# Kernel optimization log

Hardware: AMD Instinct MI355X
Metric: run time of the kernel (lower is better)

Reference implementation:

```python
import jax, jax.numpy as jnp
import numpy as np

CHEB = jnp.array([676.5203681218851, -1259.1392167224028, 771.3234287776531,
                  -176.6150291621406, 12.507343278686905, -0.13857109526572012,
                  9.984369578019572e-06, 1.5056327351493116e-07], dtype=jnp.float32)
TWO_PI = float(np.sqrt(2.0 * np.pi))  # sqrt(2*pi), matches torch two_pi constant


def _gamma(z):
    # Lanczos approximation, 8 Chebyshev terms
    x = jnp.full_like(z, 0.9999999999998099)
    for i in range(8):
        x = x + CHEB[i] / (z + (i + 1.0))
    t = z + 8.0 - 0.5
    y = TWO_PI * t ** (z + 0.5) * jnp.exp(-t) * x
    return y / z


def _lower_incl_gamma(s, x, iters=8):
    it = iters - 2
    gs = _gamma(s)
    L = x ** s * gs * jnp.exp(-x)
    gs = gs * s
    R = jnp.reciprocal(gs) * jnp.ones_like(x)
    X = x
    for k in range(it):
        gs = gs * (s + k + 1)
        R = R + X / gs
        X = X * x
    gs = gs * (s + it + 1)
    R = R + X / gs
    return L * R


def _trigamma(x):
    z = x + 1.0
    zz = z * z
    a = 0.2 - jnp.reciprocal(7.0 * zz)
    b = 1.0 - a / zz
    c = 1.0 + b / (3.0 * z)
    d = 1.0 + c / (2.0 * z)
    return d / z + jnp.reciprocal(x * x)


def _k_update(k, s):
    nm = jnp.log(k) - jax.scipy.special.digamma(k) - s
    dn = jnp.reciprocal(k) - _trigamma(k)
    return k - nm / dn


def _compute_ml_est(x, i=10):
    # x: [B, N]; returns per-image k, th of shape [B]
    x = x + 1e-07
    mean_x = jnp.mean(x, axis=1)
    s = jnp.log(mean_x) - jnp.mean(jnp.log(x), axis=1)
    s3 = s - 3.0
    rt = jnp.sqrt(s3 * s3 + 24.0 * s)
    k = (3.0 - s + rt) / (12.0 * s) + 1e-07
    for _ in range(i):
        k = _k_update(k, s)
    k = jnp.clip(k, 1e-07, 18.0)
    th = jnp.reciprocal(k) * mean_x
    return k, th


def setup_inputs() -> dict:
    key = jax.random.key(0)
    x = jax.random.uniform(key, (256, 224, 224), dtype=jnp.float32)
    return {"x": x}


def reference(x):
    B, H, W = x.shape
    xf = x.reshape(B, H * W)
    xf = xf - jnp.min(xf, axis=1, keepdims=True) + 1e-07
    k, th = _compute_ml_est(xf)            # [B], [B]
    kb = k[:, None]                         # broadcast per-image stats over pixels
    y = jnp.reciprocal(_gamma(kb)) * _lower_incl_gamma(kb, xf / th[:, None])
    y = jnp.where(jnp.isfinite(y), y, jnp.zeros_like(y))
    return y.reshape(B, H, W)
```

## Files before the change

### kernel.cpp

```cpp
#include <hip/hip_runtime.h>
#include <math.h>

#define HW   50176
#define NV4  12544
#define TPB  1024

typedef float floatx4 __attribute__((ext_vector_type(4)));

__device__ __forceinline__ float waveMin(float v) {
#pragma unroll
    for (int o = 32; o > 0; o >>= 1) v = fminf(v, __shfl_down(v, o, 64));
    return v;
}
__device__ __forceinline__ double waveSumD(double v) {
#pragma unroll
    for (int o = 32; o > 0; o >>= 1) v += __shfl_down(v, o, 64);
    return v;
}

__device__ __forceinline__ float digamma_f(float x) {
    float r = 0.0f;
#pragma unroll 6
    for (int i = 0; i < 6; ++i) {
        if (x < 6.0f) { r -= __fdividef(1.0f, x); x += 1.0f; }
    }
    float f = __fdividef(1.0f, x * x);
    float ser = f * (1.0f/12.0f - f * (1.0f/120.0f - f * (1.0f/252.0f - f * (1.0f/240.0f - f * (1.0f/132.0f)))));
    return r + logf(x) - 0.5f * __fdividef(1.0f, x) - ser;
}
__device__ __forceinline__ float trigamma_ref(float x) {
    float z = x + 1.0f, zz = z * z;
    float a = 0.2f - __fdividef(1.0f, 7.0f * zz);
    float b = 1.0f - __fdividef(a, zz);
    float c = 1.0f + __fdividef(b, 3.0f * z);
    float d = 1.0f + __fdividef(c, 2.0f * z);
    return __fdividef(d, z) + __fdividef(1.0f, x * x);
}

__global__ void __launch_bounds__(TPB)
gamma_norm2d(const float* __restrict__ x, float* __restrict__ out) {
    const int row = blockIdx.x;
    const int tid = threadIdx.x;
    const float4* __restrict__ xr = (const float4*)(x + (size_t)row * HW);

    const bool extra = (tid < (NV4 - 12 * TPB));

    float4 v[13];
#pragma unroll
    for (int j = 0; j < 12; ++j) v[j] = xr[tid + j * TPB];
    v[12] = extra ? xr[tid + 12 * TPB]
                  : make_float4(INFINITY, INFINITY, INFINITY, INFINITY);

    float pmin = INFINITY, psum = 0.0f;
#pragma unroll
    for (int j = 0; j < 13; ++j) {
        pmin = fminf(pmin, fminf(fminf(v[j].x, v[j].y), fminf(v[j].z, v[j].w)));
        if (j < 12 || extra) psum += (v[j].x + v[j].y) + (v[j].z + v[j].w);
    }
    pmin = waveMin(pmin);
    double dsum = waveSumD((double)psum);

    __shared__ float  smin[16];
    __shared__ double sacc[16];
    __shared__ float  sparams[3];
    __shared__ float  scoef[8];

    const int wid = tid >> 6, lane = tid & 63;
    if (lane == 0) { smin[wid] = pmin; sacc[wid] = dsum; }
    __syncthreads();
    if (tid == 0) {
        float mm = smin[0];
        for (int i = 1; i < 16; ++i) mm = fminf(mm, smin[i]);
        sparams[0] = mm;
    }
    __syncthreads();
    const float rmin = sparams[0];

    float psl = 0.0f;
#pragma unroll
    for (int j = 0; j < 13; ++j) {
        if (j < 12 || extra) {
            psl += (__logf(v[j].x - rmin + 1e-7f + 1e-7f) + __logf(v[j].y - rmin + 1e-7f + 1e-7f))
                 + (__logf(v[j].z - rmin + 1e-7f + 1e-7f) + __logf(v[j].w - rmin + 1e-7f + 1e-7f));
        }
    }
    double dsl = waveSumD((double)psl);
    __shared__ double ssl[16];
    if (lane == 0) ssl[wid] = dsl;
    __syncthreads();

    if (tid == 0) {
        double ts = 0.0, tl = 0.0;
        for (int i = 0; i < 16; ++i) { ts += sacc[i]; tl += ssl[i]; }
        ts -= (double)HW * ((double)rmin - 2e-7);
        const double meand = ts / (double)HW;
        float s = logf((float)meand) - (float)(tl / (double)HW);

        float s3 = s - 3.0f;
        float rt = sqrtf(s3 * s3 + 24.0f * s);
        float k  = __fdividef(3.0f - s + rt, 12.0f * s) + 1e-7f;
#pragma unroll
        for (int it = 0; it < 10; ++it) {
            float nm = logf(k) - digamma_f(k) - s;
            float dn = __fdividef(1.0f, k) - trigamma_ref(k);
            k -= __fdividef(nm, dn);
        }
        if (k < 1e-7f) k = 1e-7f;
        if (k > 18.0f) k = 18.0f;

        const double CH[8] = {676.5203681218851, -1259.1392167224028, 771.3234287776531,
                              -176.6150291621406, 12.507343278686905, -0.13857109526572012,
                              9.984369578019572e-06, 1.5056327351493116e-07};
        double acc = 0.9999999999998099;
#pragma unroll
        for (int i = 0; i < 8; ++i) acc += CH[i] / ((double)k + (double)(i + 1));
        float t  = k + 7.5f;
        float g  = __expf(fmaf(k + 0.5f, __logf(t), -t)) * 2.50662827463f * (float)acc / k;

        float den = g * k;
        scoef[0] = __fdividef(1.0f, den);
#pragma unroll
        for (int j = 1; j < 8; ++j) {
            den *= (k + (float)j);
            scoef[j] = __fdividef(1.0f, den);
        }
        sparams[1] = k;
        sparams[2] = (float)((double)k / meand);
    }
    __syncthreads();

    const float kk = sparams[1], invth = sparams[2];
    const float c0 = scoef[0], c1 = scoef[1], c2 = scoef[2], c3 = scoef[3];
    const float c4 = scoef[4], c5 = scoef[5], c6 = scoef[6], c7 = scoef[7];

    floatx4* __restrict__ yr = (floatx4*)(out + (size_t)row * HW);
#pragma unroll
    for (int j = 0; j < 13; ++j) {
        if (j < 12 || extra) {
            float e[4] = {v[j].x, v[j].y, v[j].z, v[j].w};
            floatx4 o;
#pragma unroll
            for (int q = 0; q < 4; ++q) {
                float xq = (e[q] - rmin + 1e-7f) * invth;
                float p = fmaf(c7, xq, c6);
                p = fmaf(p, xq, c5);
                p = fmaf(p, xq, c4);
                p = fmaf(p, xq, c3);
                p = fmaf(p, xq, c2);
                p = fmaf(p, xq, c1);
                p = fmaf(p, xq, c0);
                float y = __expf(fmaf(kk, __logf(xq), -xq)) * p;
                o[q] = isfinite(y) ? y : 0.0f;
            }
            __builtin_nontemporal_store(o, yr + tid + j * TPB);
        }
    }
}

extern "C" void kernel_launch(void* const* d_in, const int* in_sizes, int n_in,
                              void* d_out, int out_size, void* d_ws, size_t ws_size,
                              hipStream_t stream) {
    const float* x = (const float*)d_in[0];
    float* out = (float*)d_out;
    const int rows = in_sizes[0] / HW;
    gamma_norm2d<<<dim3(rows), dim3(TPB), 0, stream>>>(x, out);
}
```

Baseline: 110.7 us.

## Cut per-element log work, drop a barrier, and trim Newton iterations

Every thread now reduces the per-wave minima itself, which removes one __syncthreads and a shared-memory round trip. The log-sum takes one log2 of the product of four shifted values instead of four natural logs. The final pass folds the shift and scale into one fma and works in base 2 with exp2/log2. Newton iterations for k drop from 10 to 6 and the logs use fast intrinsics. The risks are overflow or underflow of the four-way product and a less converged k, both of which could change the output.

```diff
diff --git a/kernel.cpp b/kernel.cpp
--- a/kernel.cpp
+++ b/kernel.cpp
@@ -26,7 +26,7 @@
     }
     float f = __fdividef(1.0f, x * x);
     float ser = f * (1.0f/12.0f - f * (1.0f/120.0f - f * (1.0f/252.0f - f * (1.0f/240.0f - f * (1.0f/132.0f)))));
-    return r + logf(x) - 0.5f * __fdividef(1.0f, x) - ser;
+    return r + __logf(x) - 0.5f * __fdividef(1.0f, x) - ser;
 }
 __device__ __forceinline__ float trigamma_ref(float x) {
     float z = x + 1.0f, zz = z * z;
@@ -62,46 +62,45 @@
 
     __shared__ float  smin[16];
     __shared__ double sacc[16];
-    __shared__ float  sparams[3];
+    __shared__ double ssl[16];
+    __shared__ float  sparams[2];
     __shared__ float  scoef[8];
 
     const int wid = tid >> 6, lane = tid & 63;
     if (lane == 0) { smin[wid] = pmin; sacc[wid] = dsum; }
     __syncthreads();
-    if (tid == 0) {
-        float mm = smin[0];
-        for (int i = 1; i < 16; ++i) mm = fminf(mm, smin[i]);
-        sparams[0] = mm;
-    }
-    __syncthreads();
-    const float rmin = sparams[0];
 
+    float rmin = smin[0];
+#pragma unroll
+    for (int i = 1; i < 16; ++i) rmin = fminf(rmin, smin[i]);
+
+    const float C2 = rmin - 2e-7f;
     float psl = 0.0f;
 #pragma unroll
     for (int j = 0; j < 13; ++j) {
         if (j < 12 || extra) {
-            psl += (__logf(v[j].x - rmin + 1e-7f + 1e-7f) + __logf(v[j].y - rmin + 1e-7f + 1e-7f))
-                 + (__logf(v[j].z - rmin + 1e-7f + 1e-7f) + __logf(v[j].w - rmin + 1e-7f + 1e-7f));
+            float a = v[j].x - C2, b = v[j].y - C2;
+            float c = v[j].z - C2, d = v[j].w - C2;
+            psl += __log2f((a * b) * (c * d));
         }
     }
     double dsl = waveSumD((double)psl);
-    __shared__ double ssl[16];
     if (lane == 0) ssl[wid] = dsl;
     __syncthreads();
 
     if (tid == 0) {
-        double ts = 0.0, tl = 0.0;
-        for (int i = 0; i < 16; ++i) { ts += sacc[i]; tl += ssl[i]; }
+        double ts = 0.0, tl2 = 0.0;
+        for (int i = 0; i < 16; ++i) { ts += sacc[i]; tl2 += ssl[i]; }
         ts -= (double)HW * ((double)rmin - 2e-7);
         const double meand = ts / (double)HW;
-        float s = logf((float)meand) - (float)(tl / (double)HW);
+        float s = logf((float)meand) - (float)(tl2 * 0.6931471805599453 / (double)HW);
 
         float s3 = s - 3.0f;
         float rt = sqrtf(s3 * s3 + 24.0f * s);
         float k  = __fdividef(3.0f - s + rt, 12.0f * s) + 1e-7f;
 #pragma unroll
-        for (int it = 0; it < 10; ++it) {
-            float nm = logf(k) - digamma_f(k) - s;
+        for (int it = 0; it < 6; ++it) {
+            float nm = __logf(k) - digamma_f(k) - s;
             float dn = __fdividef(1.0f, k) - trigamma_ref(k);
             k -= __fdividef(nm, dn);
         }
@@ -124,14 +123,17 @@
             den *= (k + (float)j);
             scoef[j] = __fdividef(1.0f, den);
         }
-        sparams[1] = k;
-        sparams[2] = (float)((double)k / meand);
+        sparams[0] = k;
+        sparams[1] = (float)((double)k / meand);
     }
     __syncthreads();
 
-    const float kk = sparams[1], invth = sparams[2];
+    const float kk = sparams[0], invth = sparams[1];
+    const float A  = invth;
+    const float Bc = -(rmin - 1e-7f) * invth;
     const float c0 = scoef[0], c1 = scoef[1], c2 = scoef[2], c3 = scoef[3];
     const float c4 = scoef[4], c5 = scoef[5], c6 = scoef[6], c7 = scoef[7];
+    const float NL2E = -1.4426950408889634f;
 
     floatx4* __restrict__ yr = (floatx4*)(out + (size_t)row * HW);
 #pragma unroll
@@ -141,7 +143,7 @@
             floatx4 o;
 #pragma unroll
             for (int q = 0; q < 4; ++q) {
-                float xq = (e[q] - rmin + 1e-7f) * invth;
+                float xq = fmaf(e[q], A, Bc);
                 float p = fmaf(c7, xq, c6);
                 p = fmaf(p, xq, c5);
                 p = fmaf(p, xq, c4);
@@ -149,7 +151,8 @@
                 p = fmaf(p, xq, c2);
                 p = fmaf(p, xq, c1);
                 p = fmaf(p, xq, c0);
-                float y = __expf(fmaf(kk, __logf(xq), -xq)) * p;
+                float t2 = fmaf(kk, __log2f(xq), xq * NL2E);
+                float y  = __builtin_amdgcn_exp2f(t2) * p;
                 o[q] = isfinite(y) ? y : 0.0f;
             }
             __builtin_nontemporal_store(o, yr + tid + j * TPB);
```

After: 103.2 us. 6.8% less time.
